# Kernel tuning notes

Hardware: AMD Instinct MI355X
Metric: run time of the kernel (lower is better)

Reference implementation:

```python
import jax, jax.numpy as jnp
import numpy as np

N_NODES = 100000
N_EDGES = 1600000
IN_C, HID_C, OUT_C = 256, 128, 256


def setup_inputs() -> dict:
    key = jax.random.key(0)
    ks = jax.random.split(key, 8)
    x = jax.random.normal(ks[0], (N_NODES, IN_C), dtype=jnp.float32)
    src = jax.random.randint(ks[1], (N_EDGES,), 0, N_NODES, dtype=jnp.int64)
    dst = jnp.sort(jax.random.randint(ks[2], (N_EDGES,), 0, N_NODES, dtype=jnp.int64))
    # GraphConv weight [in, hid] (glorot), bias [hid]
    W_conv = jax.random.normal(ks[3], (IN_C, HID_C), dtype=jnp.float32) * (2.0 / (IN_C + HID_C)) ** 0.5
    b_conv = jnp.zeros((HID_C,), dtype=jnp.float32)
    # torch Linear weights are [out, in]
    W1 = jax.random.normal(ks[4], (HID_C, HID_C), dtype=jnp.float32) * (2.0 / (2 * HID_C)) ** 0.5
    b1 = jax.random.uniform(ks[5], (HID_C,), dtype=jnp.float32, minval=-1.0, maxval=1.0) / np.sqrt(HID_C)
    W2 = jax.random.normal(ks[6], (OUT_C, HID_C), dtype=jnp.float32) * (2.0 / (HID_C + OUT_C)) ** 0.5
    b2 = jax.random.uniform(ks[7], (OUT_C,), dtype=jnp.float32, minval=-1.0, maxval=1.0) / np.sqrt(OUT_C)
    return {"x": x, "src": src, "dst": dst, "W_conv": W_conv, "b_conv": b_conv,
            "W1": W1, "b1": b1, "W2": W2, "b2": b2}


def reference(x, src, dst, W_conv, b_conv, W1, b1, W2, b2):
    N = x.shape[0]
    ones = jnp.ones(src.shape[0], dtype=x.dtype)
    out_deg = jnp.clip(jax.ops.segment_sum(ones, src, num_segments=N), 1.0)  # [N]
    in_deg = jnp.clip(jax.ops.segment_sum(ones, dst, num_segments=N), 1.0)   # [N]
    # DGL GraphConv, norm='both', in_feats > out_feats -> weight applied before aggregation
    h = x * jax.lax.rsqrt(out_deg)[:, None]          # src-side normalization
    h = h @ W_conv                                    # [N, hid]
    m = jax.ops.segment_sum(h[src], dst, num_segments=N, indices_are_sorted=True)
    h = m * jax.lax.rsqrt(in_deg)[:, None] + b_conv   # dst-side normalization + bias
    h = jax.nn.relu(h)
    h = jax.nn.relu(h @ W1.T + b1)
    return h @ W2.T + b2
```

## Files before the change

kernel.cpp:

```cpp
#include <hip/hip_runtime.h>
#include <hip/hip_bf16.h>


typedef __attribute__((ext_vector_type(8))) short short8;
typedef __attribute__((ext_vector_type(4))) float f32x4;

static __device__ __forceinline__ float bf2f(unsigned int u16) {
    union { unsigned int i; float f; } c; c.i = u16 << 16; return c.f;
}
static __device__ __forceinline__ ushort f2bf(float f) {
    union { float f; unsigned int i; } c; c.f = f;
    unsigned int i = c.i;
    return (ushort)((i + 0x7FFFu + ((i >> 16) & 1u)) >> 16);
}

constexpr int NCHUNK   = 256;
constexpr int NBUK_MAX = 512;
constexpr int WPREP_BLOCKS = (128 * 256 + 128 * 128 + 256 * 128) / 256;

__global__ __launch_bounds__(256) void prep_kernel(
    const float* __restrict__ Wc, const float* __restrict__ W1,
    const float* __restrict__ W2, ushort* __restrict__ WcT,
    ushort* __restrict__ W1b, ushort* __restrict__ W2b,
    const int* __restrict__ src, int* __restrict__ M,
    const int* __restrict__ dst, int* __restrict__ row_ptr,
    int nE, int N, int nBuk, int chunkSz)
{
    __shared__ int cnt[NBUK_MAX];
    const int bid = blockIdx.x, tid = threadIdx.x;

    if (bid < WPREP_BLOCKS) {
        int i = bid * 256 + tid;
        if (i < 128 * 256) {
            int o = i >> 8, k = i & 255;
            WcT[o * 256 + k] = f2bf(Wc[k * 128 + o]);
        } else if (i < 128 * 256 + 128 * 128) {
            int j = i - 128 * 256;
            W1b[j] = f2bf(W1[j]);
        } else {
            int j = i - 128 * 256 - 128 * 128;
            W2b[j] = f2bf(W2[j]);
        }
        return;
    }
    if (bid < WPREP_BLOCKS + NCHUNK) {
        int c = bid - WPREP_BLOCKS;
        for (int i = tid; i < nBuk; i += 256) cnt[i] = 0;
        __syncthreads();
        int e0 = c * chunkSz, e1 = min(e0 + chunkSz, nE);
        for (int e = e0 + tid; e < e1; e += 256)
            atomicAdd(&cnt[src[e] >> 8], 1);
        __syncthreads();
        for (int b = tid; b < nBuk; b += 256)
            M[b * NCHUNK + c] = cnt[b];
        return;
    }
    int e = (bid - WPREP_BLOCKS - NCHUNK) * 256 + tid;
    if (e >= nE) return;
    int d = dst[e];
    if (e == 0) {
        for (int n = 0; n <= d; ++n) row_ptr[n] = 0;
    } else {
        int p = dst[e - 1];
        for (int n = p + 1; n <= d; ++n) row_ptr[n] = e;
    }
    if (e == nE - 1) {
        for (int n = d + 1; n <= N; ++n) row_ptr[n] = nE;
    }
}

__global__ __launch_bounds__(256) void scanA_kernel(
    int* __restrict__ M, int* __restrict__ tot)
{
    __shared__ int buf[2][NCHUNK];
    int b = blockIdx.x, tid = threadIdx.x;
    int v = M[b * NCHUNK + tid];
    buf[0][tid] = v;
    __syncthreads();
    int pi = 0;
#pragma unroll
    for (int off = 1; off < NCHUNK; off <<= 1) {
        int t = buf[pi][tid];
        if (tid >= off) t += buf[pi][tid - off];
        buf[pi ^ 1][tid] = t;
        __syncthreads();
        pi ^= 1;
    }
    int incl = buf[pi][tid];
    M[b * NCHUNK + tid] = incl - v;
    if (tid == NCHUNK - 1) tot[b] = incl;
}

__global__ __launch_bounds__(512) void scanB_kernel(
    const int* __restrict__ tot, int* __restrict__ bucket_base, int nBuk)
{
    __shared__ int t_l[NBUK_MAX], base_l[NBUK_MAX + 1];
    int tid = threadIdx.x;
    if (tid < nBuk) t_l[tid] = tot[tid];
    __syncthreads();
    if (tid == 0) {
        int base = 0;
        for (int i = 0; i < nBuk; ++i) { base_l[i] = base; base += t_l[i]; }
        base_l[nBuk] = base;
    }
    __syncthreads();
    if (tid <= nBuk) bucket_base[tid] = base_l[tid];
}

__global__ __launch_bounds__(256) void scatter_keys_kernel(
    const int* __restrict__ src, const int* __restrict__ M,
    const int* __restrict__ bucket_base, int* __restrict__ ss,
    int nE, int nBuk, int chunkSz)
{
    __shared__ int cur[NBUK_MAX];
    int c = blockIdx.x, tid = threadIdx.x;
    for (int i = tid; i < nBuk; i += 256)
        cur[i] = M[i * NCHUNK + c] + bucket_base[i];
    __syncthreads();
    int e0 = c * chunkSz, e1 = min(e0 + chunkSz, nE);
    for (int e = e0 + tid; e < e1; e += 256) {
        int s = src[e];
        int pos = atomicAdd(&cur[s >> 8], 1);
        ss[pos] = s;
    }
}

__global__ __launch_bounds__(256) void count_kernel(
    const int* __restrict__ ss, const int* __restrict__ bucket_base,
    int* __restrict__ outdeg, int N)
{
    __shared__ int hist[256];
    int b = blockIdx.x, tid = threadIdx.x;
    hist[tid] = 0;
    __syncthreads();
    int e0 = bucket_base[b], e1 = bucket_base[b + 1];
    for (int e = e0 + tid; e < e1; e += 256)
        atomicAdd(&hist[ss[e] & 255], 1);
    __syncthreads();
    int n = b * 256 + tid;
    if (n < N) outdeg[n] = hist[tid];
}

__global__ __launch_bounds__(512, 4) void gemm1_kernel(
    const float* __restrict__ A, const ushort* __restrict__ B,
    const int* __restrict__ outdeg, ushort* __restrict__ C, int nRows)
{
    __shared__ ushort Bs[128 * 256];
    __shared__ ushort As[128 * 64];
    __shared__ float rowscale[128];

    const int tid  = threadIdx.x;
    const int lane = tid & 63;
    const int w    = tid >> 6;
    const int wm   = w >> 1;
    const int wn   = w & 1;
    const int r    = lane & 15;
    const int q    = lane >> 4;
    const int row0 = blockIdx.x * 128;

    if (tid < 128) {
        int g = row0 + tid;
        int dv = (g < nRows) ? outdeg[g] : 1;
        rowscale[tid] = rsqrtf((float)max(dv, 1));
    }

#pragma unroll
    for (int s = 0; s < 8; ++s) {
        int idx = s * 512 + tid;
        int col = idx >> 5, kg = idx & 31;
        *(short8*)&Bs[col * 256 + ((kg ^ (col & 7)) * 8)] =
            *(const short8*)&B[(size_t)col * 256 + kg * 8];
    }

    int arow0 = tid >> 3,          akg0 = tid & 7;
    int arow1 = (512 + tid) >> 3,  akg1 = (512 + tid) & 7;

    float4 areg[2][2][2];

#define G1_ISSUE(cc, bb)                                                     \
    {                                                                        \
        int g0 = row0 + arow0, g1 = row0 + arow1;                            \
        areg[bb][0][0] = make_float4(0.f, 0.f, 0.f, 0.f);                    \
        areg[bb][0][1] = make_float4(0.f, 0.f, 0.f, 0.f);                    \
        areg[bb][1][0] = make_float4(0.f, 0.f, 0.f, 0.f);                    \
        areg[bb][1][1] = make_float4(0.f, 0.f, 0.f, 0.f);                    \
        if (g0 < nRows) {                                                    \
            const float* p = &A[(size_t)g0 * 256 + (cc) * 64 + akg0 * 8];    \
            areg[bb][0][0] = *(const float4*)p;                              \
            areg[bb][0][1] = *(const float4*)(p + 4);                        \
        }                                                                    \
        if (g1 < nRows) {                                                    \
            const float* p = &A[(size_t)g1 * 256 + (cc) * 64 + akg1 * 8];    \
            areg[bb][1][0] = *(const float4*)p;                              \
            areg[bb][1][1] = *(const float4*)(p + 4);                        \
        }                                                                    \
    }

    G1_ISSUE(0, 0)
    G1_ISSUE(1, 1)

    f32x4 acc[8];
#pragma unroll
    for (int t = 0; t < 8; ++t) acc[t] = (f32x4){0.f, 0.f, 0.f, 0.f};

#pragma unroll
    for (int c = 0; c < 4; ++c) {
        if (c > 0) __syncthreads();
        const int buf = c & 1;
#pragma unroll
        for (int s = 0; s < 2; ++s) {
            int arow = s ? arow1 : arow0;
            int akg  = s ? akg1  : akg0;
            float4 v0 = areg[buf][s][0], v1 = areg[buf][s][1];
            ushort u[8];
            u[0] = f2bf(v0.x); u[1] = f2bf(v0.y); u[2] = f2bf(v0.z); u[3] = f2bf(v0.w);
            u[4] = f2bf(v1.x); u[5] = f2bf(v1.y); u[6] = f2bf(v1.z); u[7] = f2bf(v1.w);
            *(short8*)&As[arow * 64 + ((akg ^ (arow & 7)) * 8)] = *(const short8*)u;
        }
        if (c + 2 < 4) G1_ISSUE(c + 2, buf)
        __syncthreads();
#pragma unroll
        for (int ks = 0; ks < 2; ++ks) {
            int sA = ks * 4 + q;
            int ra0 = wm * 32 + r, ra1 = wm * 32 + 16 + r;
            short8 a0 = *(const short8*)&As[ra0 * 64 + ((sA ^ (ra0 & 7)) * 8)];
            short8 a1 = *(const short8*)&As[ra1 * 64 + ((sA ^ (ra1 & 7)) * 8)];
            int sB = c * 8 + ks * 4 + q;
#pragma unroll
            for (int t = 0; t < 4; ++t) {
                int col = wn * 64 + t * 16 + r;
                short8 b = *(const short8*)&Bs[col * 256 + ((sB ^ (col & 7)) * 8)];
                acc[t]     = __builtin_amdgcn_mfma_f32_16x16x32_bf16(a0, b, acc[t], 0, 0, 0);
                acc[4 + t] = __builtin_amdgcn_mfma_f32_16x16x32_bf16(a1, b, acc[4 + t], 0, 0, 0);
            }
        }
    }
#undef G1_ISSUE

#pragma unroll
    for (int fr = 0; fr < 2; ++fr)
#pragma unroll
        for (int t = 0; t < 4; ++t) {
            int col = wn * 64 + t * 16 + r;
#pragma unroll
            for (int reg = 0; reg < 4; ++reg) {
                int lr = wm * 32 + fr * 16 + q * 4 + reg;
                int g = row0 + lr;
                if (g < nRows)
                    C[(size_t)g * 128 + col] = f2bf(acc[fr * 4 + t][reg] * rowscale[lr]);
            }
        }
}

__global__ __launch_bounds__(256) void gather_kernel(
    const ushort* __restrict__ h1, const int* __restrict__ src,
    const int* __restrict__ rp, const float* __restrict__ b_conv,
    ushort* __restrict__ h2, int N)
{
    int n = (blockIdx.x * 256 + threadIdx.x) >> 6;
    int lane = threadIdx.x & 63;
    if (n >= N) return;
    const int g = lane >> 4;
    const int c = lane & 15;
    int e0 = rp[n], e1 = rp[n + 1];

    float a[8];
#pragma unroll
    for (int j = 0; j < 8; ++j) a[j] = 0.f;

    int e = e0 + g;
    for (; e + 12 < e1; e += 16) {
        int s0 = src[e], s1 = src[e + 4], s2 = src[e + 8], s3 = src[e + 12];
        short8 v0 = *(const short8*)&h1[((size_t)(unsigned)s0 << 7) + c * 8];
        short8 v1 = *(const short8*)&h1[((size_t)(unsigned)s1 << 7) + c * 8];
        short8 v2 = *(const short8*)&h1[((size_t)(unsigned)s2 << 7) + c * 8];
        short8 v3 = *(const short8*)&h1[((size_t)(unsigned)s3 << 7) + c * 8];
#pragma unroll
        for (int j = 0; j < 8; ++j)
            a[j] += (bf2f((unsigned short)v0[j]) + bf2f((unsigned short)v1[j]))
                  + (bf2f((unsigned short)v2[j]) + bf2f((unsigned short)v3[j]));
    }
    for (; e < e1; e += 4) {
        short8 v0 = *(const short8*)&h1[((size_t)(unsigned)src[e] << 7) + c * 8];
#pragma unroll
        for (int j = 0; j < 8; ++j)
            a[j] += bf2f((unsigned short)v0[j]);
    }

#pragma unroll
    for (int j = 0; j < 8; ++j) {
        a[j] += __shfl_xor(a[j], 16, 64);
        a[j] += __shfl_xor(a[j], 32, 64);
    }

    if (g == 0) {
        float sc = rsqrtf((float)max(e1 - e0, 1));
        ushort o[8];
#pragma unroll
        for (int j = 0; j < 8; ++j)
            o[j] = f2bf(fmaxf(fmaf(a[j], sc, b_conv[c * 8 + j]), 0.f));
        *(short8*)&h2[((size_t)(unsigned)n << 7) + c * 8] = *(const short8*)o;
    }
}

__global__ __launch_bounds__(512, 2) void gemm23_kernel(
    const ushort* __restrict__ A, const ushort* __restrict__ W1b,
    const ushort* __restrict__ W2b, const float* __restrict__ b1,
    const float* __restrict__ b2, float* __restrict__ out, int nRows)
{
    __shared__ ushort AsTs[128 * 128];
    __shared__ ushort W1s[128 * 128];
    __shared__ ushort W2s[256 * 128];

    const int tid  = threadIdx.x;
    const int lane = tid & 63;
    const int w    = tid >> 6;
    const int wm   = w >> 1;
    const int wn   = w & 1;
    const int r    = lane & 15;
    const int q    = lane >> 4;
    const int row0 = blockIdx.x * 128;

#pragma unroll
    for (int s = 0; s < 4; ++s) {
        int idx = s * 512 + tid;
        int row = idx >> 4, kg = idx & 15;
        int g = row0 + row;
        short8 v = (short8){0, 0, 0, 0, 0, 0, 0, 0};
        if (g < nRows) v = *(const short8*)&A[(size_t)g * 128 + kg * 8];
        *(short8*)&AsTs[row * 128 + ((kg ^ (row & 7)) * 8)] = v;
    }
#pragma unroll
    for (int s = 0; s < 4; ++s) {
        int idx = s * 512 + tid;
        int col = idx >> 4, kg = idx & 15;
        *(short8*)&W1s[col * 128 + ((kg ^ (col & 7)) * 8)] =
            *(const short8*)&W1b[(size_t)col * 128 + kg * 8];
    }
#pragma unroll
    for (int s = 0; s < 8; ++s) {
        int idx = s * 512 + tid;
        int col = idx >> 4, kg = idx & 15;
        *(short8*)&W2s[col * 128 + ((kg ^ (col & 7)) * 8)] =
            *(const short8*)&W2b[(size_t)col * 128 + kg * 8];
    }
    __syncthreads();

    f32x4 acc1[8];
#pragma unroll
    for (int t = 0; t < 8; ++t) acc1[t] = (f32x4){0.f, 0.f, 0.f, 0.f};
#pragma unroll
    for (int ks = 0; ks < 4; ++ks) {
        int sA = ks * 4 + q;
        int ra0 = wm * 32 + r, ra1 = wm * 32 + 16 + r;
        short8 a0 = *(const short8*)&AsTs[ra0 * 128 + ((sA ^ (ra0 & 7)) * 8)];
        short8 a1 = *(const short8*)&AsTs[ra1 * 128 + ((sA ^ (ra1 & 7)) * 8)];
#pragma unroll
        for (int t = 0; t < 4; ++t) {
            int col = wn * 64 + t * 16 + r;
            short8 b = *(const short8*)&W1s[col * 128 + ((sA ^ (col & 7)) * 8)];
            acc1[t]     = __builtin_amdgcn_mfma_f32_16x16x32_bf16(a0, b, acc1[t], 0, 0, 0);
            acc1[4 + t] = __builtin_amdgcn_mfma_f32_16x16x32_bf16(a1, b, acc1[4 + t], 0, 0, 0);
        }
    }
    __syncthreads();

#pragma unroll
    for (int fr = 0; fr < 2; ++fr)
#pragma unroll
        for (int t = 0; t < 4; ++t) {
            int col = wn * 64 + t * 16 + r;
            float bo = b1[col];
#pragma unroll
            for (int reg = 0; reg < 4; ++reg) {
                int row = wm * 32 + fr * 16 + q * 4 + reg;
                float v = fmaxf(acc1[fr * 4 + t][reg] + bo, 0.f);
                AsTs[row * 128 + (((col >> 3) ^ (row & 7)) * 8) + (col & 7)] = f2bf(v);
            }
        }
    __syncthreads();

    f32x4 acc2[16];
#pragma unroll
    for (int t = 0; t < 16; ++t) acc2[t] = (f32x4){0.f, 0.f, 0.f, 0.f};
#pragma unroll
    for (int ks = 0; ks < 4; ++ks) {
        int sA = ks * 4 + q;
        int ra0 = wm * 32 + r, ra1 = wm * 32 + 16 + r;
        short8 a0 = *(const short8*)&AsTs[ra0 * 128 + ((sA ^ (ra0 & 7)) * 8)];
        short8 a1 = *(const short8*)&AsTs[ra1 * 128 + ((sA ^ (ra1 & 7)) * 8)];
#pragma unroll
        for (int t = 0; t < 8; ++t) {
            int col = wn * 128 + t * 16 + r;
            short8 b = *(const short8*)&W2s[col * 128 + ((sA ^ (col & 7)) * 8)];
            acc2[t]     = __builtin_amdgcn_mfma_f32_16x16x32_bf16(a0, b, acc2[t], 0, 0, 0);
            acc2[8 + t] = __builtin_amdgcn_mfma_f32_16x16x32_bf16(a1, b, acc2[8 + t], 0, 0, 0);
        }
    }

#pragma unroll
    for (int fr = 0; fr < 2; ++fr)
#pragma unroll
        for (int t = 0; t < 8; ++t) {
            int col = wn * 128 + t * 16 + r;
            float bo = b2[col];
#pragma unroll
            for (int reg = 0; reg < 4; ++reg) {
                int g = row0 + wm * 32 + fr * 16 + q * 4 + reg;
                if (g < nRows)
                    out[(size_t)g * 256 + col] = acc2[fr * 8 + t][reg] + bo;
            }
        }
}

extern "C" void kernel_launch(void* const* d_in, const int* in_sizes, int n_in,
                              void* d_out, int out_size, void* d_ws, size_t ws_size,
                              hipStream_t stream)
{
    const float* x      = (const float*)d_in[0];
    const int*   src    = (const int*)d_in[1];
    const int*   dst    = (const int*)d_in[2];
    const float* W_conv = (const float*)d_in[3];
    const float* b_conv = (const float*)d_in[4];
    const float* W1     = (const float*)d_in[5];
    const float* b1     = (const float*)d_in[6];
    const float* W2     = (const float*)d_in[7];
    const float* b2     = (const float*)d_in[8];
    float* out = (float*)d_out;

    const int N  = in_sizes[0] / 256;
    const int nE = in_sizes[1];

    const int nBuk    = (N + 255) >> 8;
    const int chunkSz = (nE + NCHUNK - 1) / NCHUNK;

    ushort* h1  = (ushort*)d_ws;
    ushort* h2  = h1 + (size_t)N * 128;
    ushort* WcT = h2 + (size_t)N * 128;
    ushort* W1b = WcT + 128 * 256;
    ushort* W2b = W1b + 128 * 128;
    int* outdeg = (int*)(W2b + 256 * 128);
    int* rp     = outdeg + N;
    int* bb     = rp + (N + 1);
    int* tot    = bb + (nBuk + 1);
    int* M      = tot + nBuk;
    int* ss     = M + nBuk * NCHUNK;

    const int rowptrBlocks = (nE + 255) / 256;
    prep_kernel<<<WPREP_BLOCKS + NCHUNK + rowptrBlocks, 256, 0, stream>>>(
        W_conv, W1, W2, WcT, W1b, W2b, src, M, dst, rp, nE, N, nBuk, chunkSz);

    scanA_kernel<<<nBuk, 256, 0, stream>>>(M, tot);
    scanB_kernel<<<1, 512, 0, stream>>>(tot, bb, nBuk);
    scatter_keys_kernel<<<NCHUNK, 256, 0, stream>>>(src, M, bb, ss, nE, nBuk, chunkSz);
    count_kernel<<<nBuk, 256, 0, stream>>>(ss, bb, outdeg, N);

    const int nBlocks128 = (N + 127) / 128;
    gemm1_kernel<<<nBlocks128, 512, 0, stream>>>(x, WcT, outdeg, h1, N);

    gather_kernel<<<(N * 64 + 255) / 256, 256, 0, stream>>>(
        h1, src, rp, b_conv, h2, N);

    gemm23_kernel<<<nBlocks128, 512, 0, stream>>>(h2, W1b, W2b, b1, b2, out, N);
}
```

Before: 184.8 us.

## Fuse gather into MLP GEMM, drop scanB, read weights directly from global

Removes the separate scanB launch by having the scatter and count kernels each compute the bucket prefix sum with a wave-level shuffle scan. The neighbor gather is moved into the gemm23 kernel, so each block aggregates its 128 destination rows straight into shared memory, and the h2 intermediate round trip disappears. Weight tiles for all GEMMs are no longer staged in LDS and are read directly from global/L2, which frees shared memory and raises occupancy (gemm23 goes to 4 blocks per SM). The cost is uncoalesced repeated weight loads and a serial per-wave gather loop of 16 nodes per wave, which may expose latency.

```diff
diff --git a/kernel.cpp b/kernel.cpp
--- a/kernel.cpp
+++ b/kernel.cpp
@@ -91,31 +91,39 @@
     if (tid == NCHUNK - 1) tot[b] = incl;
 }
 
-__global__ __launch_bounds__(512) void scanB_kernel(
-    const int* __restrict__ tot, int* __restrict__ bucket_base, int nBuk)
-{
-    __shared__ int t_l[NBUK_MAX], base_l[NBUK_MAX + 1];
-    int tid = threadIdx.x;
-    if (tid < nBuk) t_l[tid] = tot[tid];
-    __syncthreads();
-    if (tid == 0) {
+static __device__ __forceinline__ void scan_bb(
+    const int* __restrict__ tot, int* bb_l, int nBuk, int tid)
+{
+    if (tid < 64) {
         int base = 0;
-        for (int i = 0; i < nBuk; ++i) { base_l[i] = base; base += t_l[i]; }
-        base_l[nBuk] = base;
-    }
-    __syncthreads();
-    if (tid <= nBuk) bucket_base[tid] = base_l[tid];
+        for (int i0 = 0; i0 < nBuk; i0 += 64) {
+            int i = i0 + tid;
+            int v = (i < nBuk) ? tot[i] : 0;
+            int orig = v;
+#pragma unroll
+            for (int off = 1; off < 64; off <<= 1) {
+                int u = __shfl_up(v, off, 64);
+                if (tid >= off) v += u;
+            }
+            if (i < nBuk) bb_l[i] = base + v - orig;
+            base += __shfl(v, 63, 64);
+        }
+        if (tid == 0) bb_l[nBuk] = base;
+    }
+    __syncthreads();
 }
 
 __global__ __launch_bounds__(256) void scatter_keys_kernel(
     const int* __restrict__ src, const int* __restrict__ M,
-    const int* __restrict__ bucket_base, int* __restrict__ ss,
+    const int* __restrict__ tot, int* __restrict__ ss,
     int nE, int nBuk, int chunkSz)
 {
     __shared__ int cur[NBUK_MAX];
+    __shared__ int bb_l[NBUK_MAX + 1];
     int c = blockIdx.x, tid = threadIdx.x;
+    scan_bb(tot, bb_l, nBuk, tid);
     for (int i = tid; i < nBuk; i += 256)
-        cur[i] = M[i * NCHUNK + c] + bucket_base[i];
+        cur[i] = M[i * NCHUNK + c] + bb_l[i];
     __syncthreads();
     int e0 = c * chunkSz, e1 = min(e0 + chunkSz, nE);
     for (int e = e0 + tid; e < e1; e += 256) {
@@ -126,14 +134,15 @@
 }
 
 __global__ __launch_bounds__(256) void count_kernel(
-    const int* __restrict__ ss, const int* __restrict__ bucket_base,
-    int* __restrict__ outdeg, int N)
+    const int* __restrict__ ss, const int* __restrict__ tot,
+    int* __restrict__ outdeg, int N, int nBuk)
 {
     __shared__ int hist[256];
+    __shared__ int bb_l[NBUK_MAX + 1];
     int b = blockIdx.x, tid = threadIdx.x;
     hist[tid] = 0;
-    __syncthreads();
-    int e0 = bucket_base[b], e1 = bucket_base[b + 1];
+    scan_bb(tot, bb_l, nBuk, tid);
+    int e0 = bb_l[b], e1 = bb_l[b + 1];
     for (int e = e0 + tid; e < e1; e += 256)
         atomicAdd(&hist[ss[e] & 255], 1);
     __syncthreads();
@@ -145,7 +154,6 @@
     const float* __restrict__ A, const ushort* __restrict__ B,
     const int* __restrict__ outdeg, ushort* __restrict__ C, int nRows)
 {
-    __shared__ ushort Bs[128 * 256];
     __shared__ ushort As[128 * 64];
     __shared__ float rowscale[128];
 
@@ -162,14 +170,6 @@
         int g = row0 + tid;
         int dv = (g < nRows) ? outdeg[g] : 1;
         rowscale[tid] = rsqrtf((float)max(dv, 1));
-    }
-
-#pragma unroll
-    for (int s = 0; s < 8; ++s) {
-        int idx = s * 512 + tid;
-        int col = idx >> 5, kg = idx & 31;
-        *(short8*)&Bs[col * 256 + ((kg ^ (col & 7)) * 8)] =
-            *(const short8*)&B[(size_t)col * 256 + kg * 8];
     }
 
     int arow0 = tid >> 3,          akg0 = tid & 7;
@@ -229,7 +229,7 @@
 #pragma unroll
             for (int t = 0; t < 4; ++t) {
                 int col = wn * 64 + t * 16 + r;
-                short8 b = *(const short8*)&Bs[col * 256 + ((sB ^ (col & 7)) * 8)];
+                short8 b = *(const short8*)&B[(size_t)col * 256 + sB * 8];
                 acc[t]     = __builtin_amdgcn_mfma_f32_16x16x32_bf16(a0, b, acc[t], 0, 0, 0);
                 acc[4 + t] = __builtin_amdgcn_mfma_f32_16x16x32_bf16(a1, b, acc[4 + t], 0, 0, 0);
             }
@@ -252,65 +252,14 @@
         }
 }
 
-__global__ __launch_bounds__(256) void gather_kernel(
+__global__ __launch_bounds__(512, 4) void gemm23_kernel(
     const ushort* __restrict__ h1, const int* __restrict__ src,
     const int* __restrict__ rp, const float* __restrict__ b_conv,
-    ushort* __restrict__ h2, int N)
-{
-    int n = (blockIdx.x * 256 + threadIdx.x) >> 6;
-    int lane = threadIdx.x & 63;
-    if (n >= N) return;
-    const int g = lane >> 4;
-    const int c = lane & 15;
-    int e0 = rp[n], e1 = rp[n + 1];
-
-    float a[8];
-#pragma unroll
-    for (int j = 0; j < 8; ++j) a[j] = 0.f;
-
-    int e = e0 + g;
-    for (; e + 12 < e1; e += 16) {
-        int s0 = src[e], s1 = src[e + 4], s2 = src[e + 8], s3 = src[e + 12];
-        short8 v0 = *(const short8*)&h1[((size_t)(unsigned)s0 << 7) + c * 8];
-        short8 v1 = *(const short8*)&h1[((size_t)(unsigned)s1 << 7) + c * 8];
-        short8 v2 = *(const short8*)&h1[((size_t)(unsigned)s2 << 7) + c * 8];
-        short8 v3 = *(const short8*)&h1[((size_t)(unsigned)s3 << 7) + c * 8];
-#pragma unroll
-        for (int j = 0; j < 8; ++j)
-            a[j] += (bf2f((unsigned short)v0[j]) + bf2f((unsigned short)v1[j]))
-                  + (bf2f((unsigned short)v2[j]) + bf2f((unsigned short)v3[j]));
-    }
-    for (; e < e1; e += 4) {
-        short8 v0 = *(const short8*)&h1[((size_t)(unsigned)src[e] << 7) + c * 8];
-#pragma unroll
-        for (int j = 0; j < 8; ++j)
-            a[j] += bf2f((unsigned short)v0[j]);
-    }
-
-#pragma unroll
-    for (int j = 0; j < 8; ++j) {
-        a[j] += __shfl_xor(a[j], 16, 64);
-        a[j] += __shfl_xor(a[j], 32, 64);
-    }
-
-    if (g == 0) {
-        float sc = rsqrtf((float)max(e1 - e0, 1));
-        ushort o[8];
-#pragma unroll
-        for (int j = 0; j < 8; ++j)
-            o[j] = f2bf(fmaxf(fmaf(a[j], sc, b_conv[c * 8 + j]), 0.f));
-        *(short8*)&h2[((size_t)(unsigned)n << 7) + c * 8] = *(const short8*)o;
-    }
-}
-
-__global__ __launch_bounds__(512, 2) void gemm23_kernel(
-    const ushort* __restrict__ A, const ushort* __restrict__ W1b,
-    const ushort* __restrict__ W2b, const float* __restrict__ b1,
-    const float* __restrict__ b2, float* __restrict__ out, int nRows)
+    const ushort* __restrict__ W1b, const ushort* __restrict__ W2b,
+    const float* __restrict__ b1, const float* __restrict__ b2,
+    float* __restrict__ out, int N)
 {
     __shared__ ushort AsTs[128 * 128];
-    __shared__ ushort W1s[128 * 128];
-    __shared__ ushort W2s[256 * 128];
 
     const int tid  = threadIdx.x;
     const int lane = tid & 63;
@@ -321,28 +270,57 @@
     const int q    = lane >> 4;
     const int row0 = blockIdx.x * 128;
 
-#pragma unroll
-    for (int s = 0; s < 4; ++s) {
-        int idx = s * 512 + tid;
-        int row = idx >> 4, kg = idx & 15;
-        int g = row0 + row;
-        short8 v = (short8){0, 0, 0, 0, 0, 0, 0, 0};
-        if (g < nRows) v = *(const short8*)&A[(size_t)g * 128 + kg * 8];
-        *(short8*)&AsTs[row * 128 + ((kg ^ (row & 7)) * 8)] = v;
-    }
-#pragma unroll
-    for (int s = 0; s < 4; ++s) {
-        int idx = s * 512 + tid;
-        int col = idx >> 4, kg = idx & 15;
-        *(short8*)&W1s[col * 128 + ((kg ^ (col & 7)) * 8)] =
-            *(const short8*)&W1b[(size_t)col * 128 + kg * 8];
-    }
-#pragma unroll
-    for (int s = 0; s < 8; ++s) {
-        int idx = s * 512 + tid;
-        int col = idx >> 4, kg = idx & 15;
-        *(short8*)&W2s[col * 128 + ((kg ^ (col & 7)) * 8)] =
-            *(const short8*)&W2b[(size_t)col * 128 + kg * 8];
+    float bcv[8];
+    {
+        float4 bc0 = *(const float4*)&b_conv[r * 8];
+        float4 bc1 = *(const float4*)&b_conv[r * 8 + 4];
+        bcv[0] = bc0.x; bcv[1] = bc0.y; bcv[2] = bc0.z; bcv[3] = bc0.w;
+        bcv[4] = bc1.x; bcv[5] = bc1.y; bcv[6] = bc1.z; bcv[7] = bc1.w;
+    }
+#pragma unroll 1
+    for (int i = 0; i < 16; ++i) {
+        int nn = w * 16 + i;
+        int dstn = row0 + nn;
+        int e0 = 0, e1 = 0;
+        if (dstn < N) { e0 = rp[dstn]; e1 = rp[dstn + 1]; }
+
+        float a[8];
+#pragma unroll
+        for (int j = 0; j < 8; ++j) a[j] = 0.f;
+
+        int e = e0 + q;
+        for (; e + 12 < e1; e += 16) {
+            int s0 = src[e], s1 = src[e + 4], s2 = src[e + 8], s3 = src[e + 12];
+            short8 v0 = *(const short8*)&h1[((size_t)(unsigned)s0 << 7) + r * 8];
+            short8 v1 = *(const short8*)&h1[((size_t)(unsigned)s1 << 7) + r * 8];
+            short8 v2 = *(const short8*)&h1[((size_t)(unsigned)s2 << 7) + r * 8];
+            short8 v3 = *(const short8*)&h1[((size_t)(unsigned)s3 << 7) + r * 8];
+#pragma unroll
+            for (int j = 0; j < 8; ++j)
+                a[j] += (bf2f((unsigned short)v0[j]) + bf2f((unsigned short)v1[j]))
+                      + (bf2f((unsigned short)v2[j]) + bf2f((unsigned short)v3[j]));
+        }
+        for (; e < e1; e += 4) {
+            short8 v0 = *(const short8*)&h1[((size_t)(unsigned)src[e] << 7) + r * 8];
+#pragma unroll
+            for (int j = 0; j < 8; ++j)
+                a[j] += bf2f((unsigned short)v0[j]);
+        }
+
+#pragma unroll
+        for (int j = 0; j < 8; ++j) {
+            a[j] += __shfl_xor(a[j], 16, 64);
+            a[j] += __shfl_xor(a[j], 32, 64);
+        }
+
+        if (q == 0) {
+            float sc = rsqrtf((float)max(e1 - e0, 1));
+            ushort o[8];
+#pragma unroll
+            for (int j = 0; j < 8; ++j)
+                o[j] = f2bf(fmaxf(fmaf(a[j], sc, bcv[j]), 0.f));
+            *(short8*)&AsTs[nn * 128 + ((r ^ (nn & 7)) * 8)] = *(const short8*)o;
+        }
     }
     __syncthreads();
 
@@ -358,7 +336,7 @@
 #pragma unroll
         for (int t = 0; t < 4; ++t) {
             int col = wn * 64 + t * 16 + r;
-            short8 b = *(const short8*)&W1s[col * 128 + ((sA ^ (col & 7)) * 8)];
+            short8 b = *(const short8*)&W1b[(size_t)col * 128 + sA * 8];
             acc1[t]     = __builtin_amdgcn_mfma_f32_16x16x32_bf16(a0, b, acc1[t], 0, 0, 0);
             acc1[4 + t] = __builtin_amdgcn_mfma_f32_16x16x32_bf16(a1, b, acc1[4 + t], 0, 0, 0);
         }
@@ -392,7 +370,7 @@
 #pragma unroll
         for (int t = 0; t < 8; ++t) {
             int col = wn * 128 + t * 16 + r;
-            short8 b = *(const short8*)&W2s[col * 128 + ((sA ^ (col & 7)) * 8)];
+            short8 b = *(const short8*)&W2b[(size_t)col * 128 + sA * 8];
             acc2[t]     = __builtin_amdgcn_mfma_f32_16x16x32_bf16(a0, b, acc2[t], 0, 0, 0);
             acc2[8 + t] = __builtin_amdgcn_mfma_f32_16x16x32_bf16(a1, b, acc2[8 + t], 0, 0, 0);
         }
@@ -407,7 +385,7 @@
 #pragma unroll
             for (int reg = 0; reg < 4; ++reg) {
                 int g = row0 + wm * 32 + fr * 16 + q * 4 + reg;
-                if (g < nRows)
+                if (g < N)
                     out[(size_t)g * 256 + col] = acc2[fr * 8 + t][reg] + bo;
             }
         }
@@ -435,14 +413,12 @@
     const int chunkSz = (nE + NCHUNK - 1) / NCHUNK;
 
     ushort* h1  = (ushort*)d_ws;
-    ushort* h2  = h1 + (size_t)N * 128;
-    ushort* WcT = h2 + (size_t)N * 128;
+    ushort* WcT = h1 + (size_t)N * 128;
     ushort* W1b = WcT + 128 * 256;
     ushort* W2b = W1b + 128 * 128;
     int* outdeg = (int*)(W2b + 256 * 128);
     int* rp     = outdeg + N;
-    int* bb     = rp + (N + 1);
-    int* tot    = bb + (nBuk + 1);
+    int* tot    = rp + (N + 1);
     int* M      = tot + nBuk;
     int* ss     = M + nBuk * NCHUNK;
 
@@ -451,15 +427,12 @@
         W_conv, W1, W2, WcT, W1b, W2b, src, M, dst, rp, nE, N, nBuk, chunkSz);
 
     scanA_kernel<<<nBuk, 256, 0, stream>>>(M, tot);
-    scanB_kernel<<<1, 512, 0, stream>>>(tot, bb, nBuk);
-    scatter_keys_kernel<<<NCHUNK, 256, 0, stream>>>(src, M, bb, ss, nE, nBuk, chunkSz);
-    count_kernel<<<nBuk, 256, 0, stream>>>(ss, bb, outdeg, N);
+    scatter_keys_kernel<<<NCHUNK, 256, 0, stream>>>(src, M, tot, ss, nE, nBuk, chunkSz);
+    count_kernel<<<nBuk, 256, 0, stream>>>(ss, tot, outdeg, N, nBuk);
 
     const int nBlocks128 = (N + 127) / 128;
     gemm1_kernel<<<nBlocks128, 512, 0, stream>>>(x, WcT, outdeg, h1, N);
 
-    gather_kernel<<<(N * 64 + 255) / 256, 256, 0, stream>>>(
-        h1, src, rp, b_conv, h2, N);
-
-    gemm23_kernel<<<nBlocks128, 512, 0, stream>>>(h2, W1b, W2b, b1, b2, out, N);
-}
+    gemm23_kernel<<<nBlocks128, 512, 0, stream>>>(
+        h1, src, rp, b_conv, W1b, W2b, b1, b2, out, N);
+}
```

Result: slower. 234.5 us (+26.9%).
